# Optimization experiments

Hardware: AMD Instinct MI355X
Metric: run time of the kernel (lower is better)

## Reference

```python
import jax, jax.numpy as jnp
import numpy as np

N = 262144   # cohort size (k_n)
M = 8192     # number of ordinal anchor indices (len(Hj))


def setup_inputs() -> dict:
    key = jax.random.key(0)
    k1, k2, k3, k4, k5 = jax.random.split(key, 5)
    time = jax.random.uniform(k1, (N,), dtype=jnp.float32) * 1000.0
    event = (jax.random.uniform(k2, (N,), dtype=jnp.float32) < 0.3).astype(jnp.float32)
    y_true0 = jnp.stack([time, event], axis=1)          # [N,2] (time, event)
    y_true1 = y_true0                                    # second head labels (unused by loss)
    y_pred0 = jax.random.normal(k3, (N, 1), dtype=jnp.float32) * 0.1  # xbeta head 0
    y_pred1 = jax.random.normal(k4, (N, 1), dtype=jnp.float32) * 0.1  # xbeta head 1
    Hj = jnp.sort(jax.random.randint(k5, (M,), 0, N, dtype=jnp.int32))  # static event indices into sorted order
    log_vars = jnp.zeros((2, 1), dtype=jnp.float32)      # layer weights log_var0, log_var1
    return {"y_true0": y_true0, "y_true1": y_true1, "y_pred0": y_pred0,
            "y_pred1": y_pred1, "Hj": Hj, "log_vars": log_vars}


def reference(y_true0, y_true1, y_pred0, y_pred1, Hj, log_vars):
    n = y_true0.shape[0]
    # top_k with k = n == full descending sort by time
    _, order = jax.lax.top_k(y_true0[:, 0], n)

    # ---- neg_log_pl (Cox negative partial log-likelihood, per-sample vector) ----
    xbeta = y_pred0[order, 0]                 # [N] sorted by descending time
    event = y_true0[order, 1]                 # [N]
    denom = jnp.cumsum(jnp.exp(xbeta))        # risk-set cumulative sum
    lossA = -(event * (xbeta - jnp.log(denom)))  # [N]

    # ---- ordinal_loss0 (pairwise ranking over event indices Hj in sorted order) ----
    # intended math: for each j, for ii >= j: cost += 1 - exp(xbeta[Hj[j]] - xbeta[Hj[ii]])
    xb = y_pred1[order, 0]                    # [N] sorted
    xh = xb[Hj]                               # [M]
    m = Hj.shape[0]
    rec = 1.0 - jnp.exp(xh[:, None] - xh[None, :])   # [M,M] rec[j,ii]
    mask = jnp.triu(jnp.ones((m, m), dtype=bool))    # ii >= j
    cost2 = jnp.sum(jnp.where(mask, rec, 0.0))

    # ---- multi_loss combination with learned log variances ----
    lv0 = log_vars[0, 0]
    lv1 = log_vars[1, 0]
    precision1 = jnp.clip(jnp.exp(-lv1), 0.0, 1.0)
    loss = jnp.sum(lossA + lv0) + (precision1 * cost2 + lv1)
    return loss


if __name__ == "__main__":
    out = reference(**setup_inputs())
    print(out)
```

## Files before the change

### kernel.cpp

```cpp
#include <hip/hip_runtime.h>
#include <math.h>


#define BSHIFT 12
#define NBUCK (1 << 19)
#define SCAN_BLK 1024
#define NPART (NBUCK / SCAN_BLK)
#define RMAX 4
#define SEBLK 1024

__global__ void k_hist(const float2* __restrict__ yt0, int n, int rmask,
                       unsigned* __restrict__ count, unsigned* __restrict__ seq) {
  int i = blockIdx.x * blockDim.x + threadIdx.x;
  if (i >= n) return;
  int r = blockIdx.x & rmask;
  unsigned key = __float_as_uint(yt0[i].x);
  unsigned b = key >> BSHIFT;
  seq[i] = atomicAdd(&count[(size_t)r * NBUCK + b], 1u);
}

__global__ void k_scan_reduce(const unsigned* __restrict__ count, int nrep,
                              unsigned* __restrict__ countTot,
                              unsigned* __restrict__ offArr,
                              unsigned* __restrict__ cntPart) {
  __shared__ unsigned sc[SCAN_BLK];
  int t = threadIdx.x, g = blockIdx.x;
  int b = NBUCK - 1 - (g * SCAN_BLK + t);
  unsigned tot = 0;
  for (int r = 0; r < nrep; ++r) {
    offArr[(size_t)r * NBUCK + b] = tot;
    tot += count[(size_t)r * NBUCK + b];
  }
  countTot[b] = tot;
  sc[t] = tot;
  __syncthreads();
  for (int s = SCAN_BLK / 2; s > 0; s >>= 1) {
    if (t < s) sc[t] += sc[t + s];
    __syncthreads();
  }
  if (t == 0) cntPart[g] = sc[0];
}

__global__ void k_scan_final(const unsigned* __restrict__ count,
                             const unsigned* __restrict__ cntPart,
                             unsigned* __restrict__ sfxCnt) {
  __shared__ unsigned sc[SCAN_BLK];
  int t = threadIdx.x, g = blockIdx.x;
  sc[t] = (t < g) ? cntPart[t] : 0u;
  __syncthreads();
  for (int s = SCAN_BLK / 2; s > 0; s >>= 1) {
    if (t < s) sc[t] += sc[t + s];
    __syncthreads();
  }
  unsigned basC = sc[0];
  __syncthreads();
  int b = NBUCK - 1 - (g * SCAN_BLK + t);
  sc[t] = count[b];
  __syncthreads();
  for (int off = 1; off < SCAN_BLK; off <<= 1) {
    unsigned c = 0;
    if (t >= off) c = sc[t - off];
    __syncthreads();
    sc[t] += c;
    __syncthreads();
  }
  sfxCnt[b] = sc[t] + basC;
}

__global__ void k_scatter(const float2* __restrict__ yt0, const float* __restrict__ yp0, int n,
                          int rmask,
                          const unsigned* __restrict__ countTot, const unsigned* __restrict__ sfxCnt,
                          const unsigned* __restrict__ offArr, const unsigned* __restrict__ seq,
                          uint2* __restrict__ skey2, unsigned* __restrict__ sidx) {
  int i = blockIdx.x * blockDim.x + threadIdx.x;
  if (i >= n) return;
  int r = blockIdx.x & rmask;
  float2 te = yt0[i];
  unsigned key = __float_as_uint(te.x);
  unsigned ev = (te.y != 0.f) ? 0x80000000u : 0u;
  unsigned b = key >> BSHIFT;
  unsigned start = sfxCnt[b] - countTot[b];
  unsigned pos = start + offArr[(size_t)r * NBUCK + b] + seq[i];
  uint2 v; v.x = key; v.y = __float_as_uint(expf(yp0[i]));
  skey2[pos] = v;
  sidx[pos] = (unsigned)i | ev;
}

__global__ void k_scan_se(const uint2* __restrict__ skey2, int n,
                          float* __restrict__ preS, float* __restrict__ blockTot) {
  __shared__ float sf[SEBLK];
  int t = threadIdx.x;
  int p = blockIdx.x * SEBLK + t;
  float v = (p < n) ? __uint_as_float(skey2[p].y) : 0.f;
  sf[t] = v;
  __syncthreads();
  for (int off = 1; off < SEBLK; off <<= 1) {
    float a = 0.f;
    if (t >= off) a = sf[t - off];
    __syncthreads();
    sf[t] += a;
    __syncthreads();
  }
  if (p < n) preS[p] = sf[t];
  if (t == SEBLK - 1) blockTot[blockIdx.x] = sf[t];
}

__global__ void k_main(const float* __restrict__ yp1, const int* __restrict__ Hj,
                       int n, int m, int seParts,
                       const unsigned* __restrict__ countTot,
                       const unsigned* __restrict__ sfxCnt,
                       const uint2* __restrict__ skey2, const unsigned* __restrict__ sidx,
                       const float* __restrict__ preS, const float* __restrict__ blockTot,
                       float* __restrict__ xh, double* __restrict__ accum) {
  __shared__ float pb[256];
  __shared__ double red[256];
  int t = threadIdx.x;
  pb[t] = (t < seParts) ? blockTot[t] : 0.f;
  __syncthreads();
  for (int off = 1; off < 256; off <<= 1) {
    float a = 0.f;
    if (t >= off) a = pb[t - off];
    __syncthreads();
    pb[t] += a;
    __syncthreads();
  }

  int p = blockIdx.x * blockDim.x + t;
  double contrib = 0.0;
  if (p < n) {
    uint2 kv = skey2[p];
    unsigned key = kv.x;
    float e = __uint_as_float(kv.y);
    unsigned sidv = sidx[p];
    unsigned idx = sidv & 0x7FFFFFFFu;
    bool ev = (sidv >> 31) != 0u;
    unsigned b = key >> BSHIFT;
    unsigned end = sfxCnt[b];
    unsigned start = end - countTot[b];
    if (end > (unsigned)n) end = (unsigned)n;
    if (start > end) start = end;
    float wsum = 0.f;
    unsigned wcnt = 0;
    unsigned q = start;
    while (q + 8 <= end) {
      uint2 v[8];
      #pragma unroll
      for (int k = 0; k < 8; ++k) v[k] = skey2[q + k];
      #pragma unroll
      for (int k = 0; k < 8; ++k) {
        if (v[k].x > key) { wsum += __uint_as_float(v[k].y); wcnt++; }
        else if (v[k].x == key && (sidx[q + k] & 0x7FFFFFFFu) < idx) {
          wsum += __uint_as_float(v[k].y); wcnt++;
        }
      }
      q += 8;
    }
    for (; q < end; ++q) {
      uint2 v = skey2[q];
      if (v.x > key) { wsum += __uint_as_float(v.y); wcnt++; }
      else if (v.x == key && (sidx[q] & 0x7FFFFFFFu) < idx) {
        wsum += __uint_as_float(v.y); wcnt++;
      }
    }
    unsigned sb = start >> 10;
    float cross = ((sb > 0) ? pb[sb - 1] : 0.f)
                + ((start & 1023u) ? preS[start - 1] : 0.f);
    float denom = cross + wsum + e;
    int rank = (int)(start + wcnt);
    contrib = ev ? (double)logf(denom / e) : 0.0;
    int lo = 0, hi = m;
    while (lo < hi) { int mid = (lo + hi) >> 1; if (Hj[mid] < rank) lo = mid + 1; else hi = mid; }
    if (lo < m && Hj[lo] == rank) {
      float xb1 = yp1[idx];
      for (int j = lo; j < m && Hj[j] == rank; ++j) xh[j] = xb1;
    }
  }
  red[t] = contrib;
  __syncthreads();
  for (int s = 128; s > 0; s >>= 1) {
    if (t < s) red[t] += red[t + s];
    __syncthreads();
  }
  if (t == 0) atomicAdd(accum, red[0]);
}

__global__ void k_final(const float* __restrict__ xh, int m,
                        const double* __restrict__ accum, const float* __restrict__ log_vars,
                        int n, float* __restrict__ out) {
  __shared__ float wtots[16];
  __shared__ double dred[1024];
  int t = threadIdx.x;
  int lane = t & 63;
  int w = t >> 6;
  double acc = 0.0;
  float carry = 0.f;
  int passes = (m + 8191) / 8192;
  for (int pss = passes - 1; pss >= 0; --pss) {
    int base = pss * 8192 + t * 8;
    float x[8], eb[8];
    float c = 0.f;
    #pragma unroll
    for (int k = 0; k < 8; ++k) {
      int j = base + k;
      x[k] = (j < m) ? xh[j] : 0.f;
      eb[k] = (j < m) ? expf(-x[k]) : 0.f;
      c += eb[k];
    }
    float s = c;
    #pragma unroll
    for (int d = 1; d < 64; d <<= 1) {
      float o = __shfl_down(s, d, 64);
      if (lane + d < 64) s += o;
    }
    float wtot = __shfl(s, 0, 64);
    if (lane == 0) wtots[w] = wtot;
    __syncthreads();
    float after = 0.f;
    #pragma unroll
    for (int w2 = 0; w2 < 16; ++w2) if (w2 > w) after += wtots[w2];
    float ptot = 0.f;
    #pragma unroll
    for (int w2 = 0; w2 < 16; ++w2) ptot += wtots[w2];
    float S = (s - c) + after + carry;
    #pragma unroll
    for (int k = 7; k >= 0; --k) {
      int j = base + k;
      S += eb[k];
      if (j < m) acc += (double)(expf(x[k]) * S);
    }
    __syncthreads();
    carry += ptot;
  }
  dred[t] = acc;
  __syncthreads();
  for (int s2 = 512; s2 > 0; s2 >>= 1) {
    if (t < s2) dred[t] += dred[t + s2];
    __syncthreads();
  }
  if (t == 0) {
    double T = (double)m * (double)(m + 1) * 0.5;
    double cost2 = T - dred[0];
    float lv0 = log_vars[0], lv1 = log_vars[1];
    float prec1 = fminf(expf(-lv1), 1.0f);
    double loss = *accum + (double)n * (double)lv0 + (double)prec1 * cost2 + (double)lv1;
    out[0] = (float)loss;
  }
}

extern "C" void kernel_launch(void* const* d_in, const int* in_sizes, int n_in,
                              void* d_out, int out_size, void* d_ws, size_t ws_size,
                              hipStream_t stream) {
  const float2* yt0 = (const float2*)d_in[0];
  const float*  yp0 = (const float*)d_in[2];
  const float*  yp1 = (const float*)d_in[3];
  const int*    Hj  = (const int*)d_in[4];
  const float*  lv  = (const float*)d_in[5];
  int n = in_sizes[0] / 2;
  int m = in_sizes[4];
  int seParts = (n + SEBLK - 1) / SEBLK;

  int nrep = RMAX;
  {
    size_t need = (size_t)nrep * NBUCK * 4 * 2
                + (size_t)NBUCK * 4 * 2
                + (size_t)NPART * 4
                + (size_t)n * 4 * 5
                + 1024 * 4
                + (size_t)m * 4 + 256;
    if (ws_size < need) nrep = 1;
  }
  int rmask = nrep - 1;

  char* ws = (char*)d_ws;
  size_t off = 0;
  unsigned* count  = (unsigned*)(ws + off); off += (size_t)nrep * NBUCK * 4;
  double*   accum  = (double*)(ws + off);   off += 16;
  size_t zbytes = off;
  unsigned* offArr  = (unsigned*)(ws + off); off += (size_t)nrep * NBUCK * 4;
  unsigned* countTot= (unsigned*)(ws + off); off += (size_t)NBUCK * 4;
  unsigned* cntPart = (unsigned*)(ws + off); off += (size_t)NPART * 4;
  unsigned* sfxCnt  = (unsigned*)(ws + off); off += (size_t)NBUCK * 4;
  unsigned* seq     = (unsigned*)(ws + off); off += (size_t)n * 4;
  uint2*    skey2   = (uint2*)(ws + off);    off += (size_t)n * 8;
  unsigned* sidx    = (unsigned*)(ws + off); off += (size_t)n * 4;
  float*    preS    = (float*)(ws + off);    off += (size_t)n * 4;
  float*    blockTot= (float*)(ws + off);    off += 1024 * 4;
  float*    xh      = (float*)(ws + off);    off += (size_t)m * 4;

  hipMemsetAsync(d_ws, 0, zbytes, stream);

  int blk = 256;
  int g_n = (n + blk - 1) / blk;
  k_hist<<<g_n, blk, 0, stream>>>(yt0, n, rmask, count, seq);
  k_scan_reduce<<<NPART, SCAN_BLK, 0, stream>>>(count, nrep, countTot, offArr, cntPart);
  k_scan_final<<<NPART, SCAN_BLK, 0, stream>>>(countTot, cntPart, sfxCnt);
  k_scatter<<<g_n, blk, 0, stream>>>(yt0, yp0, n, rmask, countTot, sfxCnt, offArr, seq,
                                     skey2, sidx);
  k_scan_se<<<seParts, SEBLK, 0, stream>>>(skey2, n, preS, blockTot);
  k_main<<<g_n, blk, 0, stream>>>(yp1, Hj, n, m, seParts, countTot, sfxCnt,
                                  skey2, sidx, preS, blockTot, xh, accum);
  k_final<<<1, 1024, 0, stream>>>(xh, m, accum, lv, n, (float*)d_out);
}
```

Measured before the change: 139.6 us.

## Fuse sort, scans, and loss stages into one cooperative persistent kernel

```diff
diff --git a/kernel.cpp b/kernel.cpp
--- a/kernel.cpp
+++ b/kernel.cpp
@@ -1,255 +1,286 @@
 #include <hip/hip_runtime.h>
+#include <hip/hip_cooperative_groups.h>
 #include <math.h>
+
+namespace cg = cooperative_groups;
 
 
 #define BSHIFT 12
 #define NBUCK (1 << 19)
-#define SCAN_BLK 1024
-#define NPART (NBUCK / SCAN_BLK)
-#define RMAX 4
-#define SEBLK 1024
-
-__global__ void k_hist(const float2* __restrict__ yt0, int n, int rmask,
-                       unsigned* __restrict__ count, unsigned* __restrict__ seq) {
-  int i = blockIdx.x * blockDim.x + threadIdx.x;
-  if (i >= n) return;
-  int r = blockIdx.x & rmask;
-  unsigned key = __float_as_uint(yt0[i].x);
-  unsigned b = key >> BSHIFT;
-  seq[i] = atomicAdd(&count[(size_t)r * NBUCK + b], 1u);
-}
-
-__global__ void k_scan_reduce(const unsigned* __restrict__ count, int nrep,
-                              unsigned* __restrict__ countTot,
-                              unsigned* __restrict__ offArr,
-                              unsigned* __restrict__ cntPart) {
-  __shared__ unsigned sc[SCAN_BLK];
-  int t = threadIdx.x, g = blockIdx.x;
-  int b = NBUCK - 1 - (g * SCAN_BLK + t);
-  unsigned tot = 0;
-  for (int r = 0; r < nrep; ++r) {
-    offArr[(size_t)r * NBUCK + b] = tot;
-    tot += count[(size_t)r * NBUCK + b];
-  }
-  countTot[b] = tot;
-  sc[t] = tot;
-  __syncthreads();
-  for (int s = SCAN_BLK / 2; s > 0; s >>= 1) {
-    if (t < s) sc[t] += sc[t + s];
-    __syncthreads();
-  }
-  if (t == 0) cntPart[g] = sc[0];
-}
-
-__global__ void k_scan_final(const unsigned* __restrict__ count,
-                             const unsigned* __restrict__ cntPart,
-                             unsigned* __restrict__ sfxCnt) {
-  __shared__ unsigned sc[SCAN_BLK];
-  int t = threadIdx.x, g = blockIdx.x;
-  sc[t] = (t < g) ? cntPart[t] : 0u;
-  __syncthreads();
-  for (int s = SCAN_BLK / 2; s > 0; s >>= 1) {
-    if (t < s) sc[t] += sc[t + s];
-    __syncthreads();
-  }
-  unsigned basC = sc[0];
-  __syncthreads();
-  int b = NBUCK - 1 - (g * SCAN_BLK + t);
-  sc[t] = count[b];
-  __syncthreads();
-  for (int off = 1; off < SCAN_BLK; off <<= 1) {
-    unsigned c = 0;
-    if (t >= off) c = sc[t - off];
-    __syncthreads();
-    sc[t] += c;
-    __syncthreads();
-  }
-  sfxCnt[b] = sc[t] + basC;
-}
-
-__global__ void k_scatter(const float2* __restrict__ yt0, const float* __restrict__ yp0, int n,
-                          int rmask,
-                          const unsigned* __restrict__ countTot, const unsigned* __restrict__ sfxCnt,
-                          const unsigned* __restrict__ offArr, const unsigned* __restrict__ seq,
-                          uint2* __restrict__ skey2, unsigned* __restrict__ sidx) {
-  int i = blockIdx.x * blockDim.x + threadIdx.x;
-  if (i >= n) return;
-  int r = blockIdx.x & rmask;
-  float2 te = yt0[i];
-  unsigned key = __float_as_uint(te.x);
-  unsigned ev = (te.y != 0.f) ? 0x80000000u : 0u;
-  unsigned b = key >> BSHIFT;
-  unsigned start = sfxCnt[b] - countTot[b];
-  unsigned pos = start + offArr[(size_t)r * NBUCK + b] + seq[i];
-  uint2 v; v.x = key; v.y = __float_as_uint(expf(yp0[i]));
-  skey2[pos] = v;
-  sidx[pos] = (unsigned)i | ev;
-}
-
-__global__ void k_scan_se(const uint2* __restrict__ skey2, int n,
-                          float* __restrict__ preS, float* __restrict__ blockTot) {
-  __shared__ float sf[SEBLK];
-  int t = threadIdx.x;
-  int p = blockIdx.x * SEBLK + t;
-  float v = (p < n) ? __uint_as_float(skey2[p].y) : 0.f;
-  sf[t] = v;
-  __syncthreads();
-  for (int off = 1; off < SEBLK; off <<= 1) {
-    float a = 0.f;
-    if (t >= off) a = sf[t - off];
-    __syncthreads();
-    sf[t] += a;
-    __syncthreads();
-  }
-  if (p < n) preS[p] = sf[t];
-  if (t == SEBLK - 1) blockTot[blockIdx.x] = sf[t];
-}
-
-__global__ void k_main(const float* __restrict__ yp1, const int* __restrict__ Hj,
-                       int n, int m, int seParts,
-                       const unsigned* __restrict__ countTot,
-                       const unsigned* __restrict__ sfxCnt,
-                       const uint2* __restrict__ skey2, const unsigned* __restrict__ sidx,
-                       const float* __restrict__ preS, const float* __restrict__ blockTot,
-                       float* __restrict__ xh, double* __restrict__ accum) {
-  __shared__ float pb[256];
-  __shared__ double red[256];
-  int t = threadIdx.x;
-  pb[t] = (t < seParts) ? blockTot[t] : 0.f;
-  __syncthreads();
-  for (int off = 1; off < 256; off <<= 1) {
-    float a = 0.f;
-    if (t >= off) a = pb[t - off];
-    __syncthreads();
-    pb[t] += a;
-    __syncthreads();
-  }
-
-  int p = blockIdx.x * blockDim.x + t;
-  double contrib = 0.0;
-  if (p < n) {
-    uint2 kv = skey2[p];
-    unsigned key = kv.x;
-    float e = __uint_as_float(kv.y);
-    unsigned sidv = sidx[p];
-    unsigned idx = sidv & 0x7FFFFFFFu;
-    bool ev = (sidv >> 31) != 0u;
-    unsigned b = key >> BSHIFT;
-    unsigned end = sfxCnt[b];
-    unsigned start = end - countTot[b];
-    if (end > (unsigned)n) end = (unsigned)n;
-    if (start > end) start = end;
-    float wsum = 0.f;
-    unsigned wcnt = 0;
-    unsigned q = start;
-    while (q + 8 <= end) {
-      uint2 v[8];
-      #pragma unroll
-      for (int k = 0; k < 8; ++k) v[k] = skey2[q + k];
+#define NREP 4
+#define GRID 512
+#define BLK 256
+#define TOT (GRID * BLK)
+#define BPB (NBUCK / GRID)
+#define BPT (BPB / BLK)
+
+__global__ void __launch_bounds__(BLK, 2)
+k_fused(const float2* __restrict__ yt0, const float* __restrict__ yp0,
+        const float* __restrict__ yp1, const int* __restrict__ Hj,
+        const float* __restrict__ lv, int n, int m,
+        unsigned* __restrict__ count, unsigned* __restrict__ E,
+        unsigned* __restrict__ bTot, uint2* __restrict__ skey2,
+        unsigned* __restrict__ sidx, float* __restrict__ preS,
+        float* __restrict__ seTot, float* __restrict__ xh,
+        double* __restrict__ accum, float* __restrict__ out)
+{
+  cg::grid_group grid = cg::this_grid();
+  const int t = threadIdx.x;
+  const int g = blockIdx.x;
+  const int gtid = g * BLK + t;
+
+  __shared__ unsigned su[BLK];
+  __shared__ float    sf[BLK];
+  __shared__ float    pb[GRID];
+  __shared__ double   sd[BLK];
+  __shared__ float    wt[4];
+
+  {
+    uint4 z; z.x = 0u; z.y = 0u; z.z = 0u; z.w = 0u;
+    uint4* cp = (uint4*)count;
+    #pragma unroll
+    for (int k = 0; k < (NBUCK * NREP / 4) / TOT; ++k)
+      cp[(size_t)k * TOT + gtid] = z;
+    if (gtid == 0) *accum = 0.0;
+  }
+  grid.sync();
+
+  const int r = g & (NREP - 1);
+  unsigned keyR[2]; float seR[2]; unsigned seqR[2]; unsigned evR[2];
+  #pragma unroll
+  for (int el = 0; el < 2; ++el) {
+    int i = gtid + el * TOT;
+    keyR[el] = 0u; seR[el] = 0.f; seqR[el] = 0u; evR[el] = 0u;
+    if (i < n) {
+      float2 te = yt0[i];
+      unsigned key = __float_as_uint(te.x);
+      keyR[el] = key;
+      evR[el] = (te.y != 0.f) ? 0x80000000u : 0u;
+      seR[el] = expf(yp0[i]);
+      unsigned b = key >> BSHIFT;
+      seqR[el] = atomicAdd(&count[(size_t)b * NREP + r], 1u);
+    }
+  }
+  grid.sync();
+
+  unsigned incl[BPT]; unsigned thrBase; 
+  {
+    unsigned run = 0u;
+    #pragma unroll
+    for (int k = 0; k < BPT; ++k) {
+      int b = g * BPB + t * BPT + k;
+      uint4 c = ((const uint4*)count)[b];
+      run += c.x + c.y + c.z + c.w;
+      incl[k] = run;
+    }
+    su[t] = run;
+    __syncthreads();
+    for (int off = 1; off < BLK; off <<= 1) {
+      unsigned v = (t >= off) ? su[t - off] : 0u;
+      __syncthreads();
+      su[t] += v;
+      __syncthreads();
+    }
+    thrBase = (t > 0) ? su[t - 1] : 0u;
+    if (t == BLK - 1) bTot[g] = su[t];
+  }
+  grid.sync();
+
+  {
+    unsigned part = 0u;
+    for (int j = t; j < g; j += BLK) part += bTot[j];
+    su[t] = part;
+    __syncthreads();
+    for (int s = 128; s > 0; s >>= 1) { if (t < s) su[t] += su[t + s]; __syncthreads(); }
+    unsigned bBase = su[0];
+    __syncthreads();
+    unsigned e0 = bBase + thrBase;
+    uint4 ev4;
+    ev4.x = e0;
+    ev4.y = e0 + incl[0];
+    ev4.z = e0 + incl[1];
+    ev4.w = e0 + incl[2];
+    ((uint4*)E)[g * (BPB / 4) + t] = ev4;
+  }
+  grid.sync();
+
+  #pragma unroll
+  for (int el = 0; el < 2; ++el) {
+    int i = gtid + el * TOT;
+    if (i < n) {
+      unsigned key = keyR[el];
+      unsigned b = key >> BSHIFT;
+      uint4 c = ((const uint4*)count)[b];
+      unsigned cnt = c.x + c.y + c.z + c.w;
+      unsigned offr = 0u;
+      if (r > 0) offr += c.x;
+      if (r > 1) offr += c.y;
+      if (r > 2) offr += c.z;
+      unsigned start = (unsigned)n - E[b] - cnt;
+      unsigned pos = start + offr + seqR[el];
+      uint2 v; v.x = key; v.y = __float_as_uint(seR[el]);
+      skey2[pos] = v;
+      sidx[pos] = (unsigned)i | evR[el];
+    }
+  }
+  grid.sync();
+
+  {
+    int base = g * (2 * BLK);
+    int p0 = base + 2 * t, p1 = p0 + 1;
+    float e0 = (p0 < n) ? __uint_as_float(skey2[p0].y) : 0.f;
+    float e1 = (p1 < n) ? __uint_as_float(skey2[p1].y) : 0.f;
+    float pair = e0 + e1;
+    sf[t] = pair;
+    __syncthreads();
+    for (int off = 1; off < BLK; off <<= 1) {
+      float v = (t >= off) ? sf[t - off] : 0.f;
+      __syncthreads();
+      sf[t] += v;
+      __syncthreads();
+    }
+    float ex = sf[t] - pair;
+    if (p0 < n) preS[p0] = ex + e0;
+    if (p1 < n) preS[p1] = ex + e0 + e1;
+    if (t == BLK - 1) seTot[g] = sf[t];
+  }
+  grid.sync();
+
+  {
+    float a0 = seTot[2 * t];
+    float a1 = seTot[2 * t + 1];
+    float pair = a0 + a1;
+    sf[t] = pair;
+    __syncthreads();
+    for (int off = 1; off < BLK; off <<= 1) {
+      float v = (t >= off) ? sf[t - off] : 0.f;
+      __syncthreads();
+      sf[t] += v;
+      __syncthreads();
+    }
+    pb[2 * t]     = sf[t] - a1;
+    pb[2 * t + 1] = sf[t];
+    __syncthreads();
+
+    double contrib = 0.0;
+    #pragma unroll
+    for (int el = 0; el < 2; ++el) {
+      int p = gtid + el * TOT;
+      if (p >= n) continue;
+      uint2 kv = skey2[p];
+      unsigned key = kv.x;
+      float e = __uint_as_float(kv.y);
+      unsigned sidv = sidx[p];
+      unsigned idx = sidv & 0x7FFFFFFFu;
+      bool evb = (sidv >> 31) != 0u;
+      unsigned b = key >> BSHIFT;
+      uint4 c4 = ((const uint4*)count)[b];
+      unsigned cnt = c4.x + c4.y + c4.z + c4.w;
+      unsigned end = (unsigned)n - E[b];
+      unsigned start = end - cnt;
+      if (end > (unsigned)n) end = (unsigned)n;
+      if (start > end) start = end;
+      float wsum = 0.f;
+      unsigned wcnt = 0u;
+      unsigned q = start;
+      while (q + 8 <= end) {
+        uint2 v[8];
+        #pragma unroll
+        for (int k = 0; k < 8; ++k) v[k] = skey2[q + k];
+        #pragma unroll
+        for (int k = 0; k < 8; ++k) {
+          if (v[k].x > key) { wsum += __uint_as_float(v[k].y); wcnt++; }
+          else if (v[k].x == key && (sidx[q + k] & 0x7FFFFFFFu) < idx) {
+            wsum += __uint_as_float(v[k].y); wcnt++;
+          }
+        }
+        q += 8;
+      }
+      for (; q < end; ++q) {
+        uint2 v = skey2[q];
+        if (v.x > key) { wsum += __uint_as_float(v.y); wcnt++; }
+        else if (v.x == key && (sidx[q] & 0x7FFFFFFFu) < idx) {
+          wsum += __uint_as_float(v.y); wcnt++;
+        }
+      }
+      unsigned sb = start >> 9;
+      float cross = ((sb > 0) ? pb[sb - 1] : 0.f)
+                  + ((start & 511u) ? preS[start - 1] : 0.f);
+      float denom = cross + wsum + e;
+      int rank = (int)(start + wcnt);
+      if (evb) contrib += (double)logf(denom / e);
+      int lo = 0, hi = m;
+      while (lo < hi) { int mid = (lo + hi) >> 1; if (Hj[mid] < rank) lo = mid + 1; else hi = mid; }
+      if (lo < m && Hj[lo] == rank) {
+        float xb1 = yp1[idx];
+        for (int j = lo; j < m && Hj[j] == rank; ++j) xh[j] = xb1;
+      }
+    }
+    sd[t] = contrib;
+    __syncthreads();
+    for (int s = 128; s > 0; s >>= 1) { if (t < s) sd[t] += sd[t + s]; __syncthreads(); }
+    if (t == 0) atomicAdd(accum, sd[0]);
+  }
+  grid.sync();
+
+  if (g != 0) return;
+  {
+    int lane = t & 63;
+    int w = t >> 6;
+    double acc = 0.0;
+    float carry = 0.f;
+    int passes = (m + 2047) / 2048;
+    for (int pss = passes - 1; pss >= 0; --pss) {
+      int base = pss * 2048 + t * 8;
+      float x[8], eb[8];
+      float c = 0.f;
       #pragma unroll
       for (int k = 0; k < 8; ++k) {
-        if (v[k].x > key) { wsum += __uint_as_float(v[k].y); wcnt++; }
-        else if (v[k].x == key && (sidx[q + k] & 0x7FFFFFFFu) < idx) {
-          wsum += __uint_as_float(v[k].y); wcnt++;
-        }
-      }
-      q += 8;
-    }
-    for (; q < end; ++q) {
-      uint2 v = skey2[q];
-      if (v.x > key) { wsum += __uint_as_float(v.y); wcnt++; }
-      else if (v.x == key && (sidx[q] & 0x7FFFFFFFu) < idx) {
-        wsum += __uint_as_float(v.y); wcnt++;
-      }
-    }
-    unsigned sb = start >> 10;
-    float cross = ((sb > 0) ? pb[sb - 1] : 0.f)
-                + ((start & 1023u) ? preS[start - 1] : 0.f);
-    float denom = cross + wsum + e;
-    int rank = (int)(start + wcnt);
-    contrib = ev ? (double)logf(denom / e) : 0.0;
-    int lo = 0, hi = m;
-    while (lo < hi) { int mid = (lo + hi) >> 1; if (Hj[mid] < rank) lo = mid + 1; else hi = mid; }
-    if (lo < m && Hj[lo] == rank) {
-      float xb1 = yp1[idx];
-      for (int j = lo; j < m && Hj[j] == rank; ++j) xh[j] = xb1;
-    }
-  }
-  red[t] = contrib;
-  __syncthreads();
-  for (int s = 128; s > 0; s >>= 1) {
-    if (t < s) red[t] += red[t + s];
-    __syncthreads();
-  }
-  if (t == 0) atomicAdd(accum, red[0]);
-}
-
-__global__ void k_final(const float* __restrict__ xh, int m,
-                        const double* __restrict__ accum, const float* __restrict__ log_vars,
-                        int n, float* __restrict__ out) {
-  __shared__ float wtots[16];
-  __shared__ double dred[1024];
-  int t = threadIdx.x;
-  int lane = t & 63;
-  int w = t >> 6;
-  double acc = 0.0;
-  float carry = 0.f;
-  int passes = (m + 8191) / 8192;
-  for (int pss = passes - 1; pss >= 0; --pss) {
-    int base = pss * 8192 + t * 8;
-    float x[8], eb[8];
-    float c = 0.f;
-    #pragma unroll
-    for (int k = 0; k < 8; ++k) {
-      int j = base + k;
-      x[k] = (j < m) ? xh[j] : 0.f;
-      eb[k] = (j < m) ? expf(-x[k]) : 0.f;
-      c += eb[k];
-    }
-    float s = c;
-    #pragma unroll
-    for (int d = 1; d < 64; d <<= 1) {
-      float o = __shfl_down(s, d, 64);
-      if (lane + d < 64) s += o;
-    }
-    float wtot = __shfl(s, 0, 64);
-    if (lane == 0) wtots[w] = wtot;
-    __syncthreads();
-    float after = 0.f;
-    #pragma unroll
-    for (int w2 = 0; w2 < 16; ++w2) if (w2 > w) after += wtots[w2];
-    float ptot = 0.f;
-    #pragma unroll
-    for (int w2 = 0; w2 < 16; ++w2) ptot += wtots[w2];
-    float S = (s - c) + after + carry;
-    #pragma unroll
-    for (int k = 7; k >= 0; --k) {
-      int j = base + k;
-      S += eb[k];
-      if (j < m) acc += (double)(expf(x[k]) * S);
-    }
-    __syncthreads();
-    carry += ptot;
-  }
-  dred[t] = acc;
-  __syncthreads();
-  for (int s2 = 512; s2 > 0; s2 >>= 1) {
-    if (t < s2) dred[t] += dred[t + s2];
-    __syncthreads();
-  }
-  if (t == 0) {
-    double T = (double)m * (double)(m + 1) * 0.5;
-    double cost2 = T - dred[0];
-    float lv0 = log_vars[0], lv1 = log_vars[1];
-    float prec1 = fminf(expf(-lv1), 1.0f);
-    double loss = *accum + (double)n * (double)lv0 + (double)prec1 * cost2 + (double)lv1;
-    out[0] = (float)loss;
+        int j = base + k;
+        x[k] = (j < m) ? xh[j] : 0.f;
+        eb[k] = (j < m) ? expf(-x[k]) : 0.f;
+        c += eb[k];
+      }
+      float s = c;
+      #pragma unroll
+      for (int d = 1; d < 64; d <<= 1) {
+        float o = __shfl_down(s, d, 64);
+        if (lane + d < 64) s += o;
+      }
+      float wtot = __shfl(s, 0, 64);
+      if (lane == 0) wt[w] = wtot;
+      __syncthreads();
+      float after = 0.f, ptot = 0.f;
+      #pragma unroll
+      for (int w2 = 0; w2 < 4; ++w2) { ptot += wt[w2]; if (w2 > w) after += wt[w2]; }
+      float S = (s - c) + after + carry;
+      #pragma unroll
+      for (int k = 7; k >= 0; --k) {
+        int j = base + k;
+        S += eb[k];
+        if (j < m) acc += (double)(expf(x[k]) * S);
+      }
+      __syncthreads();
+      carry += ptot;
+    }
+    sd[t] = acc;
+    __syncthreads();
+    for (int s2 = 128; s2 > 0; s2 >>= 1) { if (t < s2) sd[t] += sd[t + s2]; __syncthreads(); }
+    if (t == 0) {
+      double T = (double)m * (double)(m + 1) * 0.5;
+      double cost2 = T - sd[0];
+      float lv0 = lv[0], lv1 = lv[1];
+      float prec1 = fminf(expf(-lv1), 1.0f);
+      double loss = *accum + (double)n * (double)lv0 + (double)prec1 * cost2 + (double)lv1;
+      out[0] = (float)loss;
+    }
   }
 }
 
 extern "C" void kernel_launch(void* const* d_in, const int* in_sizes, int n_in,
                               void* d_out, int out_size, void* d_ws, size_t ws_size,
                               hipStream_t stream) {
+  (void)n_in; (void)out_size;
   const float2* yt0 = (const float2*)d_in[0];
   const float*  yp0 = (const float*)d_in[2];
   const float*  yp1 = (const float*)d_in[3];
@@ -257,47 +288,28 @@
   const float*  lv  = (const float*)d_in[5];
   int n = in_sizes[0] / 2;
   int m = in_sizes[4];
-  int seParts = (n + SEBLK - 1) / SEBLK;
-
-  int nrep = RMAX;
-  {
-    size_t need = (size_t)nrep * NBUCK * 4 * 2
-                + (size_t)NBUCK * 4 * 2
-                + (size_t)NPART * 4
-                + (size_t)n * 4 * 5
-                + 1024 * 4
-                + (size_t)m * 4 + 256;
-    if (ws_size < need) nrep = 1;
-  }
-  int rmask = nrep - 1;
 
   char* ws = (char*)d_ws;
   size_t off = 0;
-  unsigned* count  = (unsigned*)(ws + off); off += (size_t)nrep * NBUCK * 4;
-  double*   accum  = (double*)(ws + off);   off += 16;
-  size_t zbytes = off;
-  unsigned* offArr  = (unsigned*)(ws + off); off += (size_t)nrep * NBUCK * 4;
-  unsigned* countTot= (unsigned*)(ws + off); off += (size_t)NBUCK * 4;
-  unsigned* cntPart = (unsigned*)(ws + off); off += (size_t)NPART * 4;
-  unsigned* sfxCnt  = (unsigned*)(ws + off); off += (size_t)NBUCK * 4;
-  unsigned* seq     = (unsigned*)(ws + off); off += (size_t)n * 4;
-  uint2*    skey2   = (uint2*)(ws + off);    off += (size_t)n * 8;
-  unsigned* sidx    = (unsigned*)(ws + off); off += (size_t)n * 4;
-  float*    preS    = (float*)(ws + off);    off += (size_t)n * 4;
-  float*    blockTot= (float*)(ws + off);    off += 1024 * 4;
-  float*    xh      = (float*)(ws + off);    off += (size_t)m * 4;
-
-  hipMemsetAsync(d_ws, 0, zbytes, stream);
-
-  int blk = 256;
-  int g_n = (n + blk - 1) / blk;
-  k_hist<<<g_n, blk, 0, stream>>>(yt0, n, rmask, count, seq);
-  k_scan_reduce<<<NPART, SCAN_BLK, 0, stream>>>(count, nrep, countTot, offArr, cntPart);
-  k_scan_final<<<NPART, SCAN_BLK, 0, stream>>>(countTot, cntPart, sfxCnt);
-  k_scatter<<<g_n, blk, 0, stream>>>(yt0, yp0, n, rmask, countTot, sfxCnt, offArr, seq,
-                                     skey2, sidx);
-  k_scan_se<<<seParts, SEBLK, 0, stream>>>(skey2, n, preS, blockTot);
-  k_main<<<g_n, blk, 0, stream>>>(yp1, Hj, n, m, seParts, countTot, sfxCnt,
-                                  skey2, sidx, preS, blockTot, xh, accum);
-  k_final<<<1, 1024, 0, stream>>>(xh, m, accum, lv, n, (float*)d_out);
+  auto alloc = [&](size_t bytes) -> void* {
+    void* p = ws + off;
+    off += (bytes + 255) & ~(size_t)255;
+    return p;
+  };
+  unsigned* count = (unsigned*)alloc((size_t)NBUCK * NREP * 4);
+  unsigned* E     = (unsigned*)alloc((size_t)NBUCK * 4);
+  unsigned* bTot  = (unsigned*)alloc((size_t)GRID * 4);
+  uint2*    skey2 = (uint2*)alloc((size_t)n * 8);
+  unsigned* sidx  = (unsigned*)alloc((size_t)n * 4);
+  float*    preS  = (float*)alloc((size_t)n * 4);
+  float*    seTot = (float*)alloc((size_t)GRID * 4);
+  float*    xh    = (float*)alloc((size_t)m * 4);
+  double*   accum = (double*)alloc(16);
+  if (off > ws_size) return;
+
+  float* outp = (float*)d_out;
+  void* args[] = { &yt0, &yp0, &yp1, &Hj, &lv, &n, &m,
+                   &count, &E, &bTot, &skey2, &sidx, &preS, &seTot, &xh,
+                   &accum, &outp };
+  hipLaunchCooperativeKernel(k_fused, dim3(GRID), dim3(BLK), args, 0, stream);
 }
```

Result: slower. 533.6 us (+282.2%).
